# Kernel tuning notes

Measured on AMD Instinct MI355X. Metric: run time of the kernel, lower is better.

## Reference

```python
import jax, jax.numpy as jnp
import numpy as np


def setup_inputs() -> dict:
    key = jax.random.key(0)
    k1, k2 = jax.random.split(key)
    queries = jax.random.normal(k1, (16, 1024, 256), dtype=jnp.float32)
    embedding = jax.random.normal(k2, (8192, 256), dtype=jnp.float32) * 0.02
    return {"queries": queries, "embedding": embedding}


def reference(queries, embedding):
    commitment_weight = 0.25
    # squared L2 distances: ||q||^2 + ||e||^2 - 2 q.e  -> [b, k, n]
    q_sq = jnp.sum(queries * queries, axis=-1, keepdims=True)          # [b,k,1]
    e_sq = jnp.sum(embedding * embedding, axis=-1)[None, None, :]      # [1,1,n]
    distances = q_sq + e_sq - 2.0 * jnp.einsum('bkc,nc->bkn', queries, embedding)
    code_indices = jnp.argmin(distances, axis=-1)                      # [b,k] int
    quantized = embedding[code_indices]                                # [b,k,c]
    commit_loss = jnp.mean((jax.lax.stop_gradient(queries) - quantized) ** 2)
    codebook_loss = jnp.mean((queries - jax.lax.stop_gradient(quantized)) ** 2)
    vq_loss = codebook_loss + commitment_weight * commit_loss
    # straight-through estimator
    quantized_st = queries + jax.lax.stop_gradient(quantized - queries)
    return (code_indices, quantized_st, vq_loss)
```

## Files before the change

kernel.cpp:

```cpp
#include <hip/hip_runtime.h>
#include <float.h>

typedef _Float16 half8 __attribute__((ext_vector_type(8)));
typedef _Float16 half4v __attribute__((ext_vector_type(4)));
typedef float f32x4 __attribute__((ext_vector_type(4)));

#define M_TOTAL 16384
#define N_CODES 8192
#define KDIM    256
#define BM 128
#define BN 128
#define BK 32
#define NK (KDIM / BK)
#define NB (N_CODES / BN)
#define TS 32
#define MARGIN 3.0e-3f
#define SQ_SCALE 512.0f
#define SE_SCALE 2048.0f
#define INV_PROD 1.9073486328125e-06f
#define RG 4
#define RCODES 1024
#define RNCH (N_CODES / RCODES)
#define RPB 1024
#define RM_BLOCKS 256
#define LR_BLOCKS 32

__global__ void prep_kernel(const float* __restrict__ src, _Float16* __restrict__ dst,
                            float* __restrict__ sq, float scale) {
    const int tid = threadIdx.x;
    const int row0 = blockIdx.x * 4;
    {
        const int r = row0 + (tid >> 6);
        const int e4 = tid & 63;
        const float4 v = *(const float4*)(src + (size_t)r * KDIM + e4 * 4);
        const half4v h = {(_Float16)(v.x * scale), (_Float16)(v.y * scale),
                          (_Float16)(v.z * scale), (_Float16)(v.w * scale)};
        ((half4v*)(dst + (size_t)r * KDIM))[e4] = h;
    }
    if (tid < 64) {
        const int grp = tid >> 4;
        const int sub = tid & 15;
        const int row = row0 + grp;
        const float* p = src + (size_t)row * KDIM + (sub >> 3) * 128 + (sub & 7);
        float r;
        {
            #pragma clang fp contract(off)
            float v = p[0];
            r = v * v;
            #pragma unroll
            for (int k = 1; k < 16; k++) { const float w = p[k * 8]; r = r + w * w; }
        }
        const float t1 = r  + __shfl_xor(r,  1, 64);
        const float t2 = t1 + __shfl_xor(t1, 2, 64);
        const float t3 = t2 + __shfl_xor(t2, 4, 64);
        const float t4 = t3 + __shfl_xor(t3, 8, 64);
        if (sub == 0) sq[row] = t4;
    }
}

__global__ void transpose_kernel(const float* __restrict__ E, float* __restrict__ ET) {
    __shared__ float tile[64][65];
    const int n0 = blockIdx.x * 64;
    const int k0 = blockIdx.y * 64;
    const int tid = threadIdx.x;
    const int r = tid >> 4;
    const int c4 = tid & 15;
    #pragma unroll
    for (int p = 0; p < 4; p++) {
        const int row = p * 16 + r;
        const float4 v = *(const float4*)(E + (size_t)(n0 + row) * KDIM + k0 + c4 * 4);
        tile[row][c4 * 4 + 0] = v.x;
        tile[row][c4 * 4 + 1] = v.y;
        tile[row][c4 * 4 + 2] = v.z;
        tile[row][c4 * 4 + 3] = v.w;
    }
    __syncthreads();
    #pragma unroll
    for (int p = 0; p < 4; p++) {
        const int d = p * 16 + r;
        float4 o;
        o.x = tile[c4 * 4 + 0][d];
        o.y = tile[c4 * 4 + 1][d];
        o.z = tile[c4 * 4 + 2][d];
        o.w = tile[c4 * 4 + 3][d];
        *(float4*)(ET + (size_t)(k0 + d) * N_CODES + n0 + c4 * 4) = o;
    }
}

union SMemU {
    _Float16 t[2][2][BM * TS];
    struct { unsigned k1[BM][2]; unsigned k2[BM][2]; } red;
};

__global__ __launch_bounds__(256, 2)
void mfma_top2_kernel(const _Float16* __restrict__ Qh, const _Float16* __restrict__ Eh,
                      const float* __restrict__ esq,
                      unsigned* __restrict__ k1s, unsigned* __restrict__ k2s) {
    __shared__ SMemU sm;
    const int tid = threadIdx.x;
    const int m0 = blockIdx.x * BM;
    const int n0 = blockIdx.y * BN;
    const int w = tid >> 6, lane = tid & 63;
    const int wm = w >> 1, wn = w & 1;
    const int qd = lane >> 4, c = lane & 15;
    const int which = w >> 1, half = w & 1;
    const _Float16* src = (which == 0) ? (Qh + (size_t)(m0 + half * 64) * KDIM)
                                       : (Eh + (size_t)(n0 + half * 64) * KDIM);
    const int hofs = half * 64 * TS;

    int srow[4], scol[4];
    #pragma unroll
    for (int it = 0; it < 4; it++) {
        const int u = it * 64 + lane;
        srow[it] = u >> 2;
        scol[it] = u & 3;
    }

    f32x4 acc[4][4];
    const f32x4 zero = {0.f, 0.f, 0.f, 0.f};
    #pragma unroll
    for (int mt = 0; mt < 4; mt++)
        #pragma unroll
        for (int nt = 0; nt < 4; nt++) acc[mt][nt] = zero;

    const int csw = (c >> 1) & 3;

    half8 pf[4];
    #pragma unroll
    for (int it = 0; it < 4; it++)
        pf[it] = *(const half8*)(src + (size_t)srow[it] * KDIM + scol[it] * 8);
    {
        _Float16* d0 = sm.t[0][which] + hofs;
        #pragma unroll
        for (int it = 0; it < 4; it++)
            *(half8*)(d0 + srow[it] * TS + (scol[it] ^ ((srow[it] >> 1) & 3)) * 8) = pf[it];
    }
    __syncthreads();

    for (int ki = 0; ki < NK; ki++) {
        if (ki + 1 < NK) {
            const int k0 = (ki + 1) * BK;
            #pragma unroll
            for (int it = 0; it < 4; it++)
                pf[it] = *(const half8*)(src + (size_t)srow[it] * KDIM + k0 + scol[it] * 8);
        }
        const _Float16* bq = sm.t[ki & 1][0];
        const _Float16* be = sm.t[ki & 1][1];
        half8 qa[4];
        #pragma unroll
        for (int mt = 0; mt < 4; mt++)
            qa[mt] = *(const half8*)(bq + (wm * 64 + mt * 16 + c) * TS + (qd ^ csw) * 8);
        #pragma unroll
        for (int nt = 0; nt < 4; nt++) {
            const half8 eh = *(const half8*)(be + (wn * 64 + nt * 16 + c) * TS + (qd ^ csw) * 8);
            #pragma unroll
            for (int mt = 0; mt < 4; mt++)
                acc[mt][nt] = __builtin_amdgcn_mfma_f32_16x16x32_f16(qa[mt], eh, acc[mt][nt], 0, 0, 0);
        }
        if (ki + 1 < NK) {
            _Float16* dn = sm.t[(ki + 1) & 1][which] + hofs;
            #pragma unroll
            for (int it = 0; it < 4; it++)
                *(half8*)(dn + srow[it] * TS + (scol[it] ^ ((srow[it] >> 1) & 3)) * 8) = pf[it];
            __syncthreads();
        }
    }

    float es8[4];
    #pragma unroll
    for (int nt = 0; nt < 4; nt++) es8[nt] = esq[n0 + wn * 64 + nt * 16 + c] + 8.0f;

    unsigned k1[16], k2[16];
    #pragma unroll
    for (int i = 0; i < 16; i++) { k1[i] = 0xFFFFFFFFu; k2[i] = 0xFFFFFFFFu; }

    #pragma unroll
    for (int mt = 0; mt < 4; mt++)
        #pragma unroll
        for (int nt = 0; nt < 4; nt++) {
            const unsigned nl = (unsigned)(wn * 64 + nt * 16 + c);
            #pragma unroll
            for (int r = 0; r < 4; r++) {
                const int i = mt * 4 + r;
                const float d = fmaf(acc[mt][nt][r], -INV_PROD, es8[nt]);
                const unsigned k = (__float_as_uint(d) & 0xFFFFFF80u) | nl;
                const unsigned t = min(k1[i], k);
                k2[i] = min(k2[i], max(k1[i], k));
                k1[i] = t;
            }
        }
    #pragma unroll
    for (int s = 1; s < 16; s <<= 1) {
        #pragma unroll
        for (int i = 0; i < 16; i++) {
            const unsigned ok1 = (unsigned)__shfl_xor((int)k1[i], s, 64);
            const unsigned ok2 = (unsigned)__shfl_xor((int)k2[i], s, 64);
            const unsigned t = min(k1[i], ok1);
            k2[i] = min(min(k2[i], ok2), max(k1[i], ok1));
            k1[i] = t;
        }
    }
    __syncthreads();
    if (c == 0) {
        #pragma unroll
        for (int mt = 0; mt < 4; mt++)
            #pragma unroll
            for (int r = 0; r < 4; r++) {
                const int ml = wm * 64 + mt * 16 + qd * 4 + r;
                sm.red.k1[ml][wn] = k1[mt * 4 + r];
                sm.red.k2[ml][wn] = k2[mt * 4 + r];
            }
    }
    __syncthreads();
    if (tid < BM) {
        const unsigned a1 = sm.red.k1[tid][0], b1 = sm.red.k1[tid][1];
        const unsigned a2 = sm.red.k2[tid][0], b2 = sm.red.k2[tid][1];
        const size_t o = (size_t)(m0 + tid) * NB + blockIdx.y;
        k1s[o] = min(a1, b1);
        k2s[o] = min(min(a2, b2), max(a1, b1));
    }
}

__global__ void finalize_kernel(const float* __restrict__ Q, const float* __restrict__ E,
                                const unsigned* __restrict__ k1s, const unsigned* __restrict__ k2s,
                                int* __restrict__ fcount, int* __restrict__ flist,
                                float* __restrict__ ws_loss, float* __restrict__ out) {
    const int q = blockIdx.x * 4 + (threadIdx.x >> 6);
    const int lane = threadIdx.x & 63;
    const unsigned k1 = k1s[(size_t)q * NB + lane];
    const unsigned k2 = k2s[(size_t)q * NB + lane];
    float v1 = __uint_as_float(k1 & 0xFFFFFF80u);
    int   gi = lane * 128 + (int)(k1 & 127u);
    float v2 = __uint_as_float(k2 & 0xFFFFFF80u);
    #pragma unroll
    for (int s = 1; s < 64; s <<= 1) {
        const float ov1 = __shfl_xor(v1, s, 64);
        const int   ogi = __shfl_xor(gi, s, 64);
        const float ov2 = __shfl_xor(v2, s, 64);
        const float nv2 = fminf(fminf(v2, ov2), fmaxf(v1, ov1));
        const bool take = (ov1 < v1) || (ov1 == v1 && ogi < gi);
        v1 = take ? ov1 : v1;
        gi = take ? ogi : gi;
        v2 = nv2;
    }
    if ((v2 - v1) < MARGIN) {
        if (lane == 0) flist[atomicAdd(fcount, 1)] = q;
        return;
    }

    if (lane == 0) out[q] = (float)gi;
    const float4 qv = *(const float4*)(Q + (size_t)q * KDIM + lane * 4);
    const float4 ev = *(const float4*)(E + (size_t)gi * KDIM + lane * 4);
    float4 st;
    {
        #pragma clang fp contract(off)
        st.x = qv.x + (ev.x - qv.x);
        st.y = qv.y + (ev.y - qv.y);
        st.z = qv.z + (ev.z - qv.z);
        st.w = qv.w + (ev.w - qv.w);
    }
    *(float4*)(out + M_TOTAL + (size_t)q * KDIM + lane * 4) = st;

    const float dx = qv.x - ev.x, dy = qv.y - ev.y, dz = qv.z - ev.z, dw = qv.w - ev.w;
    float s = dx * dx + dy * dy + dz * dz + dw * dw;
    #pragma unroll
    for (int off = 32; off > 0; off >>= 1) s += __shfl_down(s, off);
    if (lane == 0) ws_loss[q] = s;
}

__global__ __launch_bounds__(256, 4)
void refine_partial_kernel(const float* __restrict__ Q, const float* __restrict__ ET,
                           const float* __restrict__ qsq, const float* __restrict__ esq,
                           const int* __restrict__ fcount, const int* __restrict__ flist,
                           float* __restrict__ rp_v, int* __restrict__ rp_i) {
    const int cnt = *fcount;
    if (cnt == 0) return;
    const int ngroups = (cnt + RG - 1) / RG;
    const int ntasks = ngroups * RNCH;
    const int tid = threadIdx.x;
    const int w = tid >> 6, lane = tid & 63;
    __shared__ float qs[RG][KDIM];
    __shared__ float redv[4][RG];
    __shared__ int   redi[4][RG];

    for (int t = blockIdx.x; t < ntasks; t += RPB) {
        const int grp = t >> 3;
        const int chunk = t & (RNCH - 1);
        __syncthreads();
        {
            const int g = tid >> 6, c4 = tid & 63;
            const int fi = min(grp * RG + g, cnt - 1);
            const int q = flist[fi];
            *(float4*)&qs[g][c4 * 4] = *(const float4*)(Q + (size_t)q * KDIM + c4 * 4);
        }
        __syncthreads();

        const int nb = chunk * RCODES + tid * 4;
        float a[RG][4];
        #pragma unroll
        for (int g = 0; g < RG; g++)
            #pragma unroll
            for (int j = 0; j < 4; j++) a[g][j] = 0.f;

        for (int k4 = 0; k4 < KDIM / 4; k4++) {
            float4 qv[RG];
            #pragma unroll
            for (int g = 0; g < RG; g++) qv[g] = *(const float4*)&qs[g][k4 * 4];
            #pragma unroll
            for (int kk = 0; kk < 4; kk++) {
                const float4 ev = *(const float4*)(ET + (size_t)(k4 * 4 + kk) * N_CODES + nb);
                #pragma unroll
                for (int g = 0; g < RG; g++) {
                    const float qk = (kk == 0) ? qv[g].x : (kk == 1) ? qv[g].y
                                   : (kk == 2) ? qv[g].z : qv[g].w;
                    a[g][0] = fmaf(qk, ev.x, a[g][0]);
                    a[g][1] = fmaf(qk, ev.y, a[g][1]);
                    a[g][2] = fmaf(qk, ev.z, a[g][2]);
                    a[g][3] = fmaf(qk, ev.w, a[g][3]);
                }
            }
        }

        float es[4];
        #pragma unroll
        for (int j = 0; j < 4; j++) es[j] = esq[nb + j];

        #pragma unroll
        for (int g = 0; g < RG; g++) {
            const int fi = min(grp * RG + g, cnt - 1);
            const float qsv = qsq[flist[fi]];
            float bv = FLT_MAX; int bi = 0x7fffffff;
            #pragma unroll
            for (int j = 0; j < 4; j++) {
                float d;
                {
                    #pragma clang fp contract(off)
                    const float t1 = qsv + es[j];
                    d = t1 - 2.0f * a[g][j];
                }
                if (d < bv) { bv = d; bi = nb + j; }
            }
            #pragma unroll
            for (int s = 1; s < 64; s <<= 1) {
                const float ov = __shfl_xor(bv, s, 64);
                const int   oi = __shfl_xor(bi, s, 64);
                if (ov < bv || (ov == bv && oi < bi)) { bv = ov; bi = oi; }
            }
            if (lane == 0) { redv[w][g] = bv; redi[w][g] = bi; }
        }
        __syncthreads();
        if (tid < RG) {
            float fv = redv[0][tid]; int fidx = redi[0][tid];
            #pragma unroll
            for (int u = 1; u < 4; u++) {
                if (redv[u][tid] < fv || (redv[u][tid] == fv && redi[u][tid] < fidx)) {
                    fv = redv[u][tid]; fidx = redi[u][tid];
                }
            }
            rp_v[(size_t)t * RG + tid] = fv;
            rp_i[(size_t)t * RG + tid] = fidx;
        }
    }
}

__global__ void refine_merge_kernel(const float* __restrict__ Q, const float* __restrict__ E,
                                    const int* __restrict__ fcount, const int* __restrict__ flist,
                                    const float* __restrict__ rp_v, const int* __restrict__ rp_i,
                                    float* __restrict__ ws_loss, float* __restrict__ out) {
    const int cnt = *fcount;
    const int lane = threadIdx.x;
    for (int fi = blockIdx.x; fi < cnt; fi += RM_BLOCKS) {
        const int q = flist[fi];
        const int grp = fi >> 2, g = fi & 3;
        float bv = FLT_MAX; int bi = 0x7fffffff;
        if (lane < RNCH) {
            const size_t t = (size_t)(grp * RNCH + lane);
            bv = rp_v[t * RG + g];
            bi = rp_i[t * RG + g];
        }
        #pragma unroll
        for (int s = 1; s < 64; s <<= 1) {
            const float ov = __shfl_xor(bv, s, 64);
            const int   oi = __shfl_xor(bi, s, 64);
            if (ov < bv || (ov == bv && oi < bi)) { bv = ov; bi = oi; }
        }
        if (lane == 0) out[q] = (float)bi;

        const float4 qv = *(const float4*)(Q + (size_t)q * KDIM + lane * 4);
        const float4 ev = *(const float4*)(E + (size_t)bi * KDIM + lane * 4);
        float4 st;
        {
            #pragma clang fp contract(off)
            st.x = qv.x + (ev.x - qv.x);
            st.y = qv.y + (ev.y - qv.y);
            st.z = qv.z + (ev.z - qv.z);
            st.w = qv.w + (ev.w - qv.w);
        }
        *(float4*)(out + M_TOTAL + (size_t)q * KDIM + lane * 4) = st;
        const float dx = qv.x - ev.x, dy = qv.y - ev.y, dz = qv.z - ev.z, dw = qv.w - ev.w;
        float s = dx * dx + dy * dy + dz * dz + dw * dw;
        #pragma unroll
        for (int off = 32; off > 0; off >>= 1) s += __shfl_down(s, off);
        if (lane == 0) ws_loss[q] = s;
    }
}

__global__ void loss_reduce_kernel(const float* __restrict__ ws_loss, float* __restrict__ out) {
    const int tid = threadIdx.x;
    float s = 0.f;
    for (int i = blockIdx.x * 256 + tid; i < M_TOTAL; i += LR_BLOCKS * 256)
        s += ws_loss[i];
    #pragma unroll
    for (int off = 32; off > 0; off >>= 1) s += __shfl_down(s, off);
    __shared__ float ws[4];
    if ((tid & 63) == 0) ws[tid >> 6] = s;
    __syncthreads();
    if (tid == 0) {
        const float tot = (ws[0] + ws[1]) + (ws[2] + ws[3]);
        atomicAdd(out + M_TOTAL + (size_t)M_TOTAL * KDIM,
                  tot * (1.25f / (float)((size_t)M_TOTAL * KDIM)));
    }
}

extern "C" void kernel_launch(void* const* d_in, const int* in_sizes, int n_in,
                              void* d_out, int out_size, void* d_ws, size_t ws_size,
                              hipStream_t stream) {
    const float* Q = (const float*)d_in[0];
    const float* E = (const float*)d_in[1];
    float* out = (float*)d_out;

    char* ws = (char*)d_ws;
    _Float16* Qh  = (_Float16*)(ws);
    _Float16* Eh  = (_Float16*)(ws + (size_t)8  * 1024 * 1024);
    float* qsq    = (float*)   (ws + (size_t)12 * 1024 * 1024);
    float* esq    = qsq + M_TOTAL;
    unsigned* k1s = (unsigned*)(ws + (size_t)13 * 1024 * 1024);
    unsigned* k2s = (unsigned*)(ws + (size_t)17 * 1024 * 1024);
    int*   fcount = (int*)     (ws + (size_t)25 * 1024 * 1024);
    int*   flist  = fcount + 64;
    float* ws_loss= (float*)   (ws + (size_t)25 * 1024 * 1024 + 512 * 1024);
    float* ET     = (float*)   (ws + (size_t)26 * 1024 * 1024);
    float* rp_v   = (float*)k1s;
    int*   rp_i   = (int*)k2s;

    hipMemsetAsync(out + M_TOTAL + (size_t)M_TOTAL * KDIM, 0, sizeof(float), stream);
    hipMemsetAsync(fcount, 0, sizeof(int), stream);

    prep_kernel<<<M_TOTAL / 4, 256, 0, stream>>>(Q, Qh, qsq, SQ_SCALE);
    prep_kernel<<<N_CODES / 4, 256, 0, stream>>>(E, Eh, esq, SE_SCALE);
    transpose_kernel<<<dim3(N_CODES / 64, KDIM / 64), 256, 0, stream>>>(E, ET);

    mfma_top2_kernel<<<dim3(M_TOTAL / BM, N_CODES / BN), 256, 0, stream>>>(
        Qh, Eh, esq, k1s, k2s);

    finalize_kernel<<<M_TOTAL / 4, 256, 0, stream>>>(Q, E, k1s, k2s, fcount, flist, ws_loss, out);
    refine_partial_kernel<<<RPB, 256, 0, stream>>>(Q, ET, qsq, esq, fcount, flist, rp_v, rp_i);
    refine_merge_kernel<<<RM_BLOCKS, 64, 0, stream>>>(Q, E, fcount, flist, rp_v, rp_i, ws_loss, out);
    loss_reduce_kernel<<<LR_BLOCKS, 256, 0, stream>>>(ws_loss, out);
}
```

Before: 245.4 us.

## Widen code tile to 256 and stage operands via direct global-to-LDS loads

Doubles the codebook tile width per block (BN 128→256), so each wave holds a 4x8 accumulator grid. This halves the number of column blocks and the partial top-2 records the finalize pass has to merge. Operand staging now uses global_load_lds, which writes straight into LDS instead of going through registers, with a pre-swizzled source address. The key packing drops one more mantissa bit to fit an 8-bit local index, and the uncertainty margin is widened to cover it, so slightly more queries take the exact fallback path. Register pressure rises, which could hurt occupancy under the 2-blocks-per-CU launch bound.

```diff
diff --git a/kernel.cpp b/kernel.cpp
--- a/kernel.cpp
+++ b/kernel.cpp
@@ -9,12 +9,12 @@
 #define N_CODES 8192
 #define KDIM    256
 #define BM 128
-#define BN 128
+#define BN 256
 #define BK 32
 #define NK (KDIM / BK)
 #define NB (N_CODES / BN)
 #define TS 32
-#define MARGIN 3.0e-3f
+#define MARGIN 3.6e-3f
 #define SQ_SCALE 512.0f
 #define SE_SCALE 2048.0f
 #define INV_PROD 1.9073486328125e-06f
@@ -88,9 +88,15 @@
 }
 
 union SMemU {
-    _Float16 t[2][2][BM * TS];
+    struct { _Float16 q[2][BM * TS]; _Float16 e[2][BN * TS]; } t;
     struct { unsigned k1[BM][2]; unsigned k2[BM][2]; } red;
 };
+
+__device__ __forceinline__ void gl_lds16(const void* g, void* lds) {
+    __builtin_amdgcn_global_load_lds(
+        (const __attribute__((address_space(1))) unsigned*)g,
+        (__attribute__((address_space(3))) unsigned*)lds, 16, 0, 0);
+}
 
 __global__ __launch_bounds__(256, 2)
 void mfma_top2_kernel(const _Float16* __restrict__ Qh, const _Float16* __restrict__ Eh,
@@ -103,72 +109,57 @@
     const int w = tid >> 6, lane = tid & 63;
     const int wm = w >> 1, wn = w & 1;
     const int qd = lane >> 4, c = lane & 15;
-    const int which = w >> 1, half = w & 1;
-    const _Float16* src = (which == 0) ? (Qh + (size_t)(m0 + half * 64) * KDIM)
-                                       : (Eh + (size_t)(n0 + half * 64) * KDIM);
-    const int hofs = half * 64 * TS;
-
-    int srow[4], scol[4];
-    #pragma unroll
-    for (int it = 0; it < 4; it++) {
-        const int u = it * 64 + lane;
-        srow[it] = u >> 2;
-        scol[it] = u & 3;
-    }
-
-    f32x4 acc[4][4];
+
+    const int lrow = lane >> 2;
+    const int gsw = (lane & 3) ^ ((lane >> 3) & 3);
+    const _Float16* qsrc = Qh + (size_t)(m0 + w * 32 + lrow) * KDIM + gsw * 8;
+    const _Float16* esrc = Eh + (size_t)(n0 + w * 64 + lrow) * KDIM + gsw * 8;
+
+    f32x4 acc[4][8];
     const f32x4 zero = {0.f, 0.f, 0.f, 0.f};
     #pragma unroll
     for (int mt = 0; mt < 4; mt++)
         #pragma unroll
-        for (int nt = 0; nt < 4; nt++) acc[mt][nt] = zero;
+        for (int nt = 0; nt < 8; nt++) acc[mt][nt] = zero;
+
+    #define STAGE(buf, kofs) do {                                                  \
+        _Float16* qdst = sm.t.q[buf] + w * 1024;                                   \
+        _Float16* edst = sm.t.e[buf] + w * 2048;                                   \
+        gl_lds16(qsrc + (kofs),             qdst);                                 \
+        gl_lds16(qsrc + 16 * KDIM + (kofs), qdst + 512);                           \
+        gl_lds16(esrc + (kofs),             edst);                                 \
+        gl_lds16(esrc + 16 * KDIM + (kofs), edst + 512);                           \
+        gl_lds16(esrc + 32 * KDIM + (kofs), edst + 1024);                          \
+        gl_lds16(esrc + 48 * KDIM + (kofs), edst + 1536);                          \
+    } while (0)
+
+    STAGE(0, 0);
+    __syncthreads();
 
     const int csw = (c >> 1) & 3;
 
-    half8 pf[4];
-    #pragma unroll
-    for (int it = 0; it < 4; it++)
-        pf[it] = *(const half8*)(src + (size_t)srow[it] * KDIM + scol[it] * 8);
-    {
-        _Float16* d0 = sm.t[0][which] + hofs;
-        #pragma unroll
-        for (int it = 0; it < 4; it++)
-            *(half8*)(d0 + srow[it] * TS + (scol[it] ^ ((srow[it] >> 1) & 3)) * 8) = pf[it];
-    }
-    __syncthreads();
-
     for (int ki = 0; ki < NK; ki++) {
-        if (ki + 1 < NK) {
-            const int k0 = (ki + 1) * BK;
-            #pragma unroll
-            for (int it = 0; it < 4; it++)
-                pf[it] = *(const half8*)(src + (size_t)srow[it] * KDIM + k0 + scol[it] * 8);
-        }
-        const _Float16* bq = sm.t[ki & 1][0];
-        const _Float16* be = sm.t[ki & 1][1];
+        if (ki + 1 < NK) STAGE((ki + 1) & 1, (ki + 1) * BK);
+        const _Float16* bq = sm.t.q[ki & 1];
+        const _Float16* be = sm.t.e[ki & 1];
         half8 qa[4];
         #pragma unroll
         for (int mt = 0; mt < 4; mt++)
             qa[mt] = *(const half8*)(bq + (wm * 64 + mt * 16 + c) * TS + (qd ^ csw) * 8);
         #pragma unroll
-        for (int nt = 0; nt < 4; nt++) {
-            const half8 eh = *(const half8*)(be + (wn * 64 + nt * 16 + c) * TS + (qd ^ csw) * 8);
+        for (int nt = 0; nt < 8; nt++) {
+            const half8 eh = *(const half8*)(be + (wn * 128 + nt * 16 + c) * TS + (qd ^ csw) * 8);
             #pragma unroll
             for (int mt = 0; mt < 4; mt++)
                 acc[mt][nt] = __builtin_amdgcn_mfma_f32_16x16x32_f16(qa[mt], eh, acc[mt][nt], 0, 0, 0);
         }
-        if (ki + 1 < NK) {
-            _Float16* dn = sm.t[(ki + 1) & 1][which] + hofs;
-            #pragma unroll
-            for (int it = 0; it < 4; it++)
-                *(half8*)(dn + srow[it] * TS + (scol[it] ^ ((srow[it] >> 1) & 3)) * 8) = pf[it];
-            __syncthreads();
-        }
-    }
-
-    float es8[4];
-    #pragma unroll
-    for (int nt = 0; nt < 4; nt++) es8[nt] = esq[n0 + wn * 64 + nt * 16 + c] + 8.0f;
+        __syncthreads();
+    }
+    #undef STAGE
+
+    float es8[8];
+    #pragma unroll
+    for (int nt = 0; nt < 8; nt++) es8[nt] = esq[n0 + wn * 128 + nt * 16 + c] + 8.0f;
 
     unsigned k1[16], k2[16];
     #pragma unroll
@@ -177,13 +168,13 @@
     #pragma unroll
     for (int mt = 0; mt < 4; mt++)
         #pragma unroll
-        for (int nt = 0; nt < 4; nt++) {
-            const unsigned nl = (unsigned)(wn * 64 + nt * 16 + c);
+        for (int nt = 0; nt < 8; nt++) {
+            const unsigned nl = (unsigned)(wn * 128 + nt * 16 + c);
             #pragma unroll
             for (int r = 0; r < 4; r++) {
                 const int i = mt * 4 + r;
                 const float d = fmaf(acc[mt][nt][r], -INV_PROD, es8[nt]);
-                const unsigned k = (__float_as_uint(d) & 0xFFFFFF80u) | nl;
+                const unsigned k = (__float_as_uint(d) & 0xFFFFFF00u) | nl;
                 const unsigned t = min(k1[i], k);
                 k2[i] = min(k2[i], max(k1[i], k));
                 k1[i] = t;
@@ -227,23 +218,28 @@
                                 float* __restrict__ ws_loss, float* __restrict__ out) {
     const int q = blockIdx.x * 4 + (threadIdx.x >> 6);
     const int lane = threadIdx.x & 63;
-    const unsigned k1 = k1s[(size_t)q * NB + lane];
-    const unsigned k2 = k2s[(size_t)q * NB + lane];
-    float v1 = __uint_as_float(k1 & 0xFFFFFF80u);
-    int   gi = lane * 128 + (int)(k1 & 127u);
-    float v2 = __uint_as_float(k2 & 0xFFFFFF80u);
+    unsigned d1 = 0xFFFFFF00u;
+    unsigned d2 = 0xFFFFFF00u;
+    int gi = 0x7FFFFFFF;
+    if (lane < NB) {
+        const unsigned k1 = k1s[(size_t)q * NB + lane];
+        const unsigned k2 = k2s[(size_t)q * NB + lane];
+        d1 = k1 & 0xFFFFFF00u;
+        gi = lane * BN + (int)(k1 & 255u);
+        d2 = k2 & 0xFFFFFF00u;
+    }
     #pragma unroll
     for (int s = 1; s < 64; s <<= 1) {
-        const float ov1 = __shfl_xor(v1, s, 64);
-        const int   ogi = __shfl_xor(gi, s, 64);
-        const float ov2 = __shfl_xor(v2, s, 64);
-        const float nv2 = fminf(fminf(v2, ov2), fmaxf(v1, ov1));
-        const bool take = (ov1 < v1) || (ov1 == v1 && ogi < gi);
-        v1 = take ? ov1 : v1;
+        const unsigned od1 = (unsigned)__shfl_xor((int)d1, s, 64);
+        const int      ogi = __shfl_xor(gi, s, 64);
+        const unsigned od2 = (unsigned)__shfl_xor((int)d2, s, 64);
+        const unsigned nd2 = min(min(d2, od2), max(d1, od1));
+        const bool take = (od1 < d1) || (od1 == d1 && ogi < gi);
+        d1 = take ? od1 : d1;
         gi = take ? ogi : gi;
-        v2 = nv2;
-    }
-    if ((v2 - v1) < MARGIN) {
+        d2 = nd2;
+    }
+    if ((__uint_as_float(d2) - __uint_as_float(d1)) < MARGIN) {
         if (lane == 0) flist[atomicAdd(fcount, 1)] = q;
         return;
     }
```

Result: faster. 224.9 us (-8.4%).
